# Performance work log

Hardware: AMD Instinct MI355X
Metric: run time of the kernel (lower is better)

The kernel has to match this reference:

```python
import jax, jax.numpy as jnp
import numpy as np

NEG_SLOPE = 0.2  # LeakyReLU slope used by PyG GATConv


def gat_conv(x, src, dst, W_src, W_dst, att_src, att_dst, bias, num_nodes):
    """Single-head PyG-style GATConv.
    x: [N, F_in]; src/dst: [E] int; W_*: [C, F_in]; att_*: [C]; bias: [C].
    """
    h_src = x @ W_src.T            # [N, C]
    h_dst = x @ W_dst.T            # [N, C]
    a_src = h_src @ att_src        # [N]
    a_dst = h_dst @ att_dst        # [N]
    e = a_src[src] + a_dst[dst]    # [E]
    e = jnp.where(e >= 0, e, NEG_SLOPE * e)  # leaky_relu
    # softmax over edges grouped by destination node
    m = jax.ops.segment_max(e, dst, num_segments=num_nodes)          # [N]
    ex = jnp.exp(e - m[dst])                                          # [E]
    denom = jax.ops.segment_sum(ex, dst, num_segments=num_nodes)      # [N]
    alpha = ex / (denom[dst] + 1e-16)                                 # [E]
    out = jax.ops.segment_sum(alpha[:, None] * h_src[src], dst,
                              num_segments=num_nodes)                 # [N, C]
    return out + bias


def setup_inputs() -> dict:
    key = jax.random.key(0)
    ks = jax.random.split(key, 16)
    N, E = 10000, 160000
    dim_in, dim_out = 4096, 20
    hid = dim_in // 4  # 1024
    x = jax.random.normal(ks[0], (N, dim_in), dtype=jnp.float32)
    edges = jax.random.randint(ks[1], (2, E), 0, N, dtype=jnp.int64)
    std = 0.01
    return {
        "x": x,
        "edges": edges,
        "W0": jax.random.normal(ks[2], (dim_out, dim_in)) * std,
        "b0": jnp.zeros((dim_out,), jnp.float32),
        "Ws1": jax.random.normal(ks[3], (hid, dim_in)) * (1.0 / np.sqrt(dim_in)),
        "Wd1": jax.random.normal(ks[4], (hid, dim_in)) * (1.0 / np.sqrt(dim_in)),
        "as1": jax.random.normal(ks[5], (hid,)) * 0.1,
        "ad1": jax.random.normal(ks[6], (hid,)) * 0.1,
        "b1": jnp.zeros((hid,), jnp.float32),
        "Ws2": jax.random.normal(ks[7], (dim_out, hid)) * (1.0 / np.sqrt(hid)),
        "Wd2": jax.random.normal(ks[8], (dim_out, hid)) * (1.0 / np.sqrt(hid)),
        "as2": jax.random.normal(ks[9], (dim_out,)) * 0.1,
        "ad2": jax.random.normal(ks[10], (dim_out,)) * 0.1,
        "b2": jnp.zeros((dim_out,), jnp.float32),
    }


def reference(x, edges, W0, b0, Ws1, Wd1, as1, ad1, b1, Ws2, Wd2, as2, ad2, b2):
    N = x.shape[0]
    # GATConv default add_self_loops=True; returned edge list includes them
    ar = jnp.arange(N, dtype=edges.dtype)
    new_edge = jnp.concatenate([edges, jnp.stack([ar, ar])], axis=1)  # [2, E+N]
    src, dst = new_edge[0], new_edge[1]

    # mil_score0: plain linear
    mil_score0 = x @ W0.T + b0                           # [N, dim_out]

    # mil_score1: two-layer GAT with ELU in between
    h = gat_conv(x, src, dst, Ws1, Wd1, as1, ad1, b1, N)  # [N, hid]
    h = jax.nn.elu(h)
    mil_score1 = gat_conv(h, src, dst, Ws2, Wd2, as2, ad2, b2, N)  # [N, dim_out]

    # softmax over proposals (dim=0) per class, fused with GAT output
    mil_score = jax.nn.softmax(mil_score0, axis=0) * mil_score1
    return (mil_score, new_edge)
```

## Files before the change

kernel.cpp:

```cpp
#include <hip/hip_runtime.h>

#define NN   10000
#define FIN  4096
#define HID  1024
#define CO   20
#define EE   160000
#define ET   170000
#define NBV  (HID + 22)

typedef __bf16 bf16x8 __attribute__((ext_vector_type(8)));
typedef float  f32x4  __attribute__((ext_vector_type(4)));

__device__ __forceinline__ float bf2f(unsigned short u) {
    unsigned int x = ((unsigned int)u) << 16;
    float f; __builtin_memcpy(&f, &x, 4); return f;
}
__device__ __forceinline__ unsigned short f2bf(float f) {
    unsigned int x; __builtin_memcpy(&x, &f, 4);
    unsigned int r = (x + 0x7fffu + ((x >> 16) & 1u)) >> 16;
    return (unsigned short)r;
}
__device__ __forceinline__ void unpack4(int2 v, float* f) {
    unsigned int a = (unsigned int)v.x, b = (unsigned int)v.y;
    f[0] = bf2f((unsigned short)(a & 0xffffu)); f[1] = bf2f((unsigned short)(a >> 16));
    f[2] = bf2f((unsigned short)(b & 0xffffu)); f[3] = bf2f((unsigned short)(b >> 16));
}
__device__ __forceinline__ int edge_at(const int* __restrict__ e, int idx, int is64) {
    return is64 ? e[2 * (size_t)idx] : e[idx];
}
__device__ __forceinline__ int4 pack8(float4 a, float4 b) {
    int4 o;
    o.x = (int)((unsigned)f2bf(a.x) | ((unsigned)f2bf(a.y) << 16));
    o.y = (int)((unsigned)f2bf(a.z) | ((unsigned)f2bf(a.w) << 16));
    o.z = (int)((unsigned)f2bf(b.x) | ((unsigned)f2bf(b.y) << 16));
    o.w = (int)((unsigned)f2bf(b.z) | ((unsigned)f2bf(b.w) << 16));
    return o;
}

__global__ void k_cast(const float* __restrict__ src, unsigned short* __restrict__ dst,
                       const int* __restrict__ edg, int* __restrict__ cnt,
                       int* __restrict__ flag) {
    int i = blockIdx.x * 256 + threadIdx.x;
    const float4* s = (const float4*)src + (size_t)i * 2;
    *(int4*)(dst + (size_t)i * 8) = pack8(s[0], s[1]);
    if (i < NN) cnt[i] = 0;
    if (i < 64) {
        int v = edg[2 * i + 1];
        unsigned long long bm = __ballot(v != 0);
        if (i == 0) flag[0] = (bm == 0ull) ? 1 : 0;
    }
}

#define BEXTB 2088
__global__ __launch_bounds__(256) void k_prep(const float* __restrict__ Ws1,
                                              const float* __restrict__ Wd1,
                                              const float* __restrict__ W0,
                                              const float* __restrict__ as1,
                                              const float* __restrict__ ad1,
                                              unsigned short* __restrict__ Bext,
                                              float* __restrict__ partS,
                                              float* __restrict__ partD) {
    if (blockIdx.x < BEXTB) {
        int i = blockIdx.x * 256 + threadIdx.x;
        int row = i >> 9;
        int col = (i & 511) * 8;
        const float* src = (row < HID) ? Ws1 + (size_t)row * FIN
                                       : W0 + (size_t)(row - HID) * FIN;
        const float4* s = (const float4*)(src + col);
        *(int4*)(Bext + (size_t)row * FIN + col) = pack8(s[0], s[1]);
    } else {
        int bx = blockIdx.x - BEXTB;
        int k = (bx & 15) * 256 + threadIdx.x;
        int chunk = bx >> 4;
        int r0 = chunk * 128;
        float s = 0.f, d = 0.f;
        for (int r = r0; r < r0 + 128; r++) {
            s += as1[r] * Ws1[(size_t)r * FIN + k];
            d += ad1[r] * Wd1[(size_t)r * FIN + k];
        }
        partS[chunk * FIN + k] = s;
        partD[chunk * FIN + k] = d;
    }
}

__global__ void k_vred(const float* __restrict__ partS, const float* __restrict__ partD,
                       const float* __restrict__ Wd2, const float* __restrict__ ad2,
                       unsigned short* __restrict__ Bext, float* __restrict__ wd2v) {
    int k = blockIdx.x * 256 + threadIdx.x;
    if (k < FIN) {
        float s = 0.f, d = 0.f;
        for (int j = 0; j < 8; j++) { s += partS[j * FIN + k]; d += partD[j * FIN + k]; }
        Bext[(size_t)(HID + CO) * FIN + k]     = f2bf(s);
        Bext[(size_t)(HID + CO + 1) * FIN + k] = f2bf(d);
    }
    if (k < HID) {
        float d2 = 0.f;
        for (int r = 0; r < CO; r++) d2 += ad2[r] * Wd2[(size_t)r * HID + k];
        wd2v[k] = d2;
    }
}

#define GBM 128
#define GBN 128
#define GBK 32
#define NMT ((NN + GBM - 1) / GBM)
#define NNT ((NBV + GBN - 1) / GBN)
#define NWG (NMT * NNT)

__global__ __launch_bounds__(256) void k_gemm_ext(
    const unsigned short* __restrict__ A, const unsigned short* __restrict__ B,
    unsigned short* __restrict__ H1, float* __restrict__ ext, int M) {
    __shared__ __bf16 As[2][GBM * GBK];
    __shared__ __bf16 Bs[2][GBN * GBK];
    int bid = blockIdx.x;
    int q = NWG >> 3, r = NWG & 7;
    int xcd = bid & 7, idx = bid >> 3;
    int swz = (xcd < r ? xcd * (q + 1) : r * (q + 1) + (xcd - r) * q) + idx;
    int mt = swz / NNT;
    int nt = swz - mt * NNT;
    int m0 = mt * GBM;
    int n0 = nt * GBN;
    int tid = threadIdx.x;
    int lane = tid & 63, wave = tid >> 6;
    int wm = (wave >> 1) * 64, wn = (wave & 1) * 64;
    int lrow = lane & 15, lk8 = (lane >> 4) * 8;

    int srow = lane >> 2;
    int scol = (lane & 3) * 8;
    int arow = wave * 32;
    int gmA0 = m0 + arow + srow;      if (gmA0 >= M) gmA0 = M - 1;
    int gmA1 = m0 + arow + 16 + srow; if (gmA1 >= M) gmA1 = M - 1;
    int gnB0 = n0 + arow + srow;      if (gnB0 >= NBV) gnB0 = NBV - 1;
    int gnB1 = n0 + arow + 16 + srow; if (gnB1 >= NBV) gnB1 = NBV - 1;
    const unsigned short* pA0 = A + (size_t)gmA0 * FIN + scol;
    const unsigned short* pA1 = A + (size_t)gmA1 * FIN + scol;
    const unsigned short* pB0 = B + (size_t)gnB0 * FIN + scol;
    const unsigned short* pB1 = B + (size_t)gnB1 * FIN + scol;

    f32x4 acc[4][4];
#pragma unroll
    for (int r2 = 0; r2 < 4; r2++)
#pragma unroll
        for (int c = 0; c < 4; c++) acc[r2][c] = (f32x4){0.f, 0.f, 0.f, 0.f};

    auto stage = [&](int buf, int k0) {
        __builtin_amdgcn_global_load_lds(
            (const __attribute__((address_space(1))) void*)(pA0 + k0),
            (__attribute__((address_space(3))) void*)&As[buf][arow * GBK], 16, 0, 0);
        __builtin_amdgcn_global_load_lds(
            (const __attribute__((address_space(1))) void*)(pA1 + k0),
            (__attribute__((address_space(3))) void*)&As[buf][(arow + 16) * GBK], 16, 0, 0);
        __builtin_amdgcn_global_load_lds(
            (const __attribute__((address_space(1))) void*)(pB0 + k0),
            (__attribute__((address_space(3))) void*)&Bs[buf][arow * GBK], 16, 0, 0);
        __builtin_amdgcn_global_load_lds(
            (const __attribute__((address_space(1))) void*)(pB1 + k0),
            (__attribute__((address_space(3))) void*)&Bs[buf][(arow + 16) * GBK], 16, 0, 0);
    };

    stage(0, 0);
    int cur = 0;
    for (int k0 = 0; k0 < FIN; k0 += GBK) {
        __syncthreads();
        if (k0 + GBK < FIN) stage(cur ^ 1, k0 + GBK);
        bf16x8 af[4], bfr[4];
#pragma unroll
        for (int r2 = 0; r2 < 4; r2++)
            af[r2] = *(const bf16x8*)(&As[cur][(wm + r2 * 16 + lrow) * GBK + lk8]);
#pragma unroll
        for (int c = 0; c < 4; c++)
            bfr[c] = *(const bf16x8*)(&Bs[cur][(wn + c * 16 + lrow) * GBK + lk8]);
#pragma unroll
        for (int r2 = 0; r2 < 4; r2++)
#pragma unroll
            for (int c = 0; c < 4; c++)
                acc[r2][c] = __builtin_amdgcn_mfma_f32_16x16x32_bf16(af[r2], bfr[c], acc[r2][c], 0, 0, 0);
        cur ^= 1;
    }
    int orow = (lane >> 4) * 4, ocol = lane & 15;
#pragma unroll
    for (int r2 = 0; r2 < 4; r2++)
#pragma unroll
        for (int c = 0; c < 4; c++)
#pragma unroll
            for (int i = 0; i < 4; i++) {
                int m = m0 + wm + r2 * 16 + orow + i;
                int n = n0 + wn + c * 16 + ocol;
                if (m < M) {
                    float v = acc[r2][c][i];
                    if (n < HID)      H1[(size_t)m * HID + n] = f2bf(v);
                    else if (n < NBV) ext[(size_t)(n - HID) * NN + m] = v;
                }
            }
}

#define CNTB 665
__global__ __launch_bounds__(256) void k_cfs(const int* __restrict__ edges,
                                             const int* __restrict__ flag,
                                             int* __restrict__ cnt,
                                             const float* __restrict__ ext,
                                             float* __restrict__ gmax,
                                             float* __restrict__ ginv) {
    if (blockIdx.x < CNTB) {
        int k = blockIdx.x * 256 + threadIdx.x;
        if (k >= ET) return;
        int is64 = flag[0];
        int d = (k < EE) ? edge_at(edges, EE + k, is64) : (k - EE);
        if ((unsigned)d < NN) atomicAdd(&cnt[d], 1);
    } else {
        int c = blockIdx.x - CNTB, t = threadIdx.x, lane = t & 63, wv = t >> 6;
        const float* row = ext + (size_t)c * NN;
        __shared__ float r4[4];
        __shared__ float bv;
        float m = -INFINITY;
        for (int n = t; n < NN; n += 256) m = fmaxf(m, row[n]);
        for (int o = 32; o; o >>= 1) m = fmaxf(m, __shfl_xor(m, o, 64));
        if (lane == 0) r4[wv] = m;
        __syncthreads();
        if (t == 0) bv = fmaxf(fmaxf(r4[0], r4[1]), fmaxf(r4[2], r4[3]));
        __syncthreads();
        float gm = bv;
        __syncthreads();
        float s = 0.f;
        for (int n = t; n < NN; n += 256) s += expf(row[n] - gm);
        for (int o = 32; o; o >>= 1) s += __shfl_xor(s, o, 64);
        if (lane == 0) r4[wv] = s;
        __syncthreads();
        if (t == 0) { gmax[c] = gm; ginv[c] = 1.0f / (r4[0] + r4[1] + r4[2] + r4[3]); }
    }
}

__global__ __launch_bounds__(1024) void k_scan(const int* __restrict__ cnt,
                                               int* __restrict__ offs,
                                               int* __restrict__ cursor) {
    int t = threadIdx.x, lane = t & 63, wv = t >> 6;
    int base = t * 10;
    int c[10]; int tot = 0;
    if (base < NN) {
#pragma unroll
        for (int j = 0; j < 10; j++) { c[j] = cnt[base + j]; tot += c[j]; }
    }
    int incl = tot;
#pragma unroll
    for (int o = 1; o < 64; o <<= 1) {
        int v = __shfl_up(incl, o, 64);
        if (lane >= o) incl += v;
    }
    __shared__ int wsum[16];
    if (lane == 63) wsum[wv] = incl;
    __syncthreads();
    if (t < 16) {
        int v = wsum[t];
        int inc2 = v;
#pragma unroll
        for (int o = 1; o < 16; o <<= 1) {
            int u = __shfl_up(inc2, o, 64);
            if (t >= o) inc2 += u;
        }
        wsum[t] = inc2 - v;
    }
    __syncthreads();
    int excl = incl - tot + wsum[wv];
    if (base < NN) {
        int run = excl;
#pragma unroll
        for (int j = 0; j < 10; j++) {
            cursor[base + j] = run;
            run += c[j];
            offs[base + j + 1] = run;
        }
    }
    if (t == 0) offs[0] = 0;
}

__global__ void k_scatter(const int* __restrict__ edges, const int* __restrict__ flag,
                          int* __restrict__ cursor, int* __restrict__ csr_src) {
    int k = blockIdx.x * 256 + threadIdx.x;
    if (k >= ET) return;
    int is64 = flag[0];
    int s, d;
    if (k < EE) { s = edge_at(edges, k, is64); d = edge_at(edges, EE + k, is64); }
    else        { s = d = k - EE; }
    if ((unsigned)d >= NN) return;
    if ((unsigned)s >= NN) s = 0;
    int pos = atomicAdd(&cursor[d], 1);
    csr_src[pos] = s;
}

__global__ __launch_bounds__(64) void k_agg1f(
    const int* __restrict__ offs, const int* __restrict__ csr,
    const float* __restrict__ a_src, const float* __restrict__ a_dst,
    const unsigned short* __restrict__ H1,
    const float* __restrict__ b1, const float* __restrict__ Ws2,
    const float* __restrict__ wd2v, const float* __restrict__ as2,
    float* __restrict__ H2, float* __restrict__ a_src2, float* __restrict__ a_dst2) {
    int n = blockIdx.x, lane = threadIdx.x;
    int b = offs[n], deg = offs[n + 1] - b;
    float ad = a_dst[n];
    __shared__ int   sc[128];
    __shared__ float av[128];
    bool small = (deg <= 128);
    float gm, inv;
    if (small) {
        float mymax = -INFINITY;
        for (int j = lane; j < deg; j += 64) {
            int s = csr[b + j];
            float v = a_src[s] + ad;
            v = (v >= 0.f) ? v : 0.2f * v;
            sc[j] = s; av[j] = v;
            mymax = fmaxf(mymax, v);
        }
        for (int o = 32; o; o >>= 1) mymax = fmaxf(mymax, __shfl_xor(mymax, o, 64));
        gm = mymax;
        float mysum = 0.f;
        for (int j = lane; j < deg; j += 64) {
            float e = expf(av[j] - gm);
            av[j] = e;
            mysum += e;
        }
        for (int o = 32; o; o >>= 1) mysum += __shfl_xor(mysum, o, 64);
        inv = 1.0f / (mysum + 1e-16f);
        for (int j = lane; j < deg; j += 64) av[j] *= inv;
        __syncthreads();
    } else {
        float mymax = -INFINITY;
        for (int j = lane; j < deg; j += 64) {
            float v = a_src[csr[b + j]] + ad;
            v = (v >= 0.f) ? v : 0.2f * v;
            mymax = fmaxf(mymax, v);
        }
        for (int o = 32; o; o >>= 1) mymax = fmaxf(mymax, __shfl_xor(mymax, o, 64));
        gm = mymax;
        float mysum = 0.f;
        for (int j = lane; j < deg; j += 64) {
            float v = a_src[csr[b + j]] + ad;
            v = (v >= 0.f) ? v : 0.2f * v;
            mysum += expf(v - gm);
        }
        for (int o = 32; o; o >>= 1) mysum += __shfl_xor(mysum, o, 64);
        inv = 1.0f / (mysum + 1e-16f);
    }
    float acc[16];
#pragma unroll
    for (int i = 0; i < 16; i++) acc[i] = 0.f;
    for (int base = 0; base < deg; base += 128) {
        int lim = deg - base; if (lim > 128) lim = 128;
        if (!small) {
            __syncthreads();
            for (int j = lane; j < lim; j += 64) {
                int s = csr[b + base + j];
                float v = a_src[s] + ad;
                v = (v >= 0.f) ? v : 0.2f * v;
                sc[j] = s; av[j] = expf(v - gm) * inv;
            }
            __syncthreads();
        }
        for (int j = 0; j < lim; j++) {
            int s = sc[j]; float w = av[j];
            const unsigned short* hp = H1 + (size_t)s * HID + lane * 8;
            int4 p0 = *(const int4*)hp;
            int4 p1 = *(const int4*)(hp + 512);
            float f[8];
            unpack4(make_int2(p0.x, p0.y), f);
            unpack4(make_int2(p0.z, p0.w), f + 4);
#pragma unroll
            for (int i = 0; i < 8; i++) acc[i] += w * f[i];
            unpack4(make_int2(p1.x, p1.y), f);
            unpack4(make_int2(p1.z, p1.w), f + 4);
#pragma unroll
            for (int i = 0; i < 8; i++) acc[8 + i] += w * f[i];
        }
    }
    float xf[16];
    {
        const float4* bp0 = (const float4*)(b1 + lane * 8);
        const float4* bp1 = (const float4*)(b1 + 512 + lane * 8);
        float4 c0 = bp0[0], c1 = bp0[1], c2 = bp1[0], c3 = bp1[1];
        float bb[16] = {c0.x,c0.y,c0.z,c0.w, c1.x,c1.y,c1.z,c1.w,
                        c2.x,c2.y,c2.z,c2.w, c3.x,c3.y,c3.z,c3.w};
#pragma unroll
        for (int i = 0; i < 16; i++) {
            float v = acc[i] + bb[i];
            xf[i] = (v > 0.f) ? v : (expf(v) - 1.f);
        }
    }
    float a2 = 0.f;
    for (int c = 0; c < 21; c++) {
        const float* wr = (c < CO) ? Ws2 + (size_t)c * HID : wd2v;
        const float4* w0 = (const float4*)(wr + lane * 8);
        const float4* w1 = (const float4*)(wr + 512 + lane * 8);
        float4 wa = w0[0], wb = w0[1], wc = w1[0], wd = w1[1];
        float dp = xf[0]*wa.x + xf[1]*wa.y + xf[2]*wa.z + xf[3]*wa.w
                 + xf[4]*wb.x + xf[5]*wb.y + xf[6]*wb.z + xf[7]*wb.w
                 + xf[8]*wc.x + xf[9]*wc.y + xf[10]*wc.z + xf[11]*wc.w
                 + xf[12]*wd.x + xf[13]*wd.y + xf[14]*wd.z + xf[15]*wd.w;
        for (int o = 32; o; o >>= 1) dp += __shfl_xor(dp, o, 64);
        if (c < CO) {
            if (lane == 0) H2[(size_t)n * CO + c] = dp;
            a2 += dp * as2[c];
        } else if (lane == 0) a_dst2[n] = dp;
    }
    if (lane == 0) a_src2[n] = a2;
}

__global__ __launch_bounds__(64) void k_agg2(const int* __restrict__ offs,
                                             const int* __restrict__ csr,
                                             const float* __restrict__ a_src,
                                             const float* __restrict__ a_dst,
                                             const float* __restrict__ H2,
                                             const float* __restrict__ b2,
                                             float* __restrict__ ms1T) {
    int n = blockIdx.x, lane = threadIdx.x;
    int b = offs[n], deg = offs[n + 1] - b;
    float ad = a_dst[n];
    __shared__ int   sc[128];
    __shared__ float av[128];
    bool small = (deg <= 128);
    float gm, inv;
    if (small) {
        float mymax = -INFINITY;
        for (int j = lane; j < deg; j += 64) {
            int s = csr[b + j];
            float v = a_src[s] + ad;
            v = (v >= 0.f) ? v : 0.2f * v;
            sc[j] = s; av[j] = v;
            mymax = fmaxf(mymax, v);
        }
        for (int o = 32; o; o >>= 1) mymax = fmaxf(mymax, __shfl_xor(mymax, o, 64));
        gm = mymax;
        float mysum = 0.f;
        for (int j = lane; j < deg; j += 64) {
            float e = expf(av[j] - gm);
            av[j] = e;
            mysum += e;
        }
        for (int o = 32; o; o >>= 1) mysum += __shfl_xor(mysum, o, 64);
        inv = 1.0f / (mysum + 1e-16f);
        for (int j = lane; j < deg; j += 64) av[j] *= inv;
        __syncthreads();
    } else {
        float mymax = -INFINITY;
        for (int j = lane; j < deg; j += 64) {
            float v = a_src[csr[b + j]] + ad;
            v = (v >= 0.f) ? v : 0.2f * v;
            mymax = fmaxf(mymax, v);
        }
        for (int o = 32; o; o >>= 1) mymax = fmaxf(mymax, __shfl_xor(mymax, o, 64));
        gm = mymax;
        float mysum = 0.f;
        for (int j = lane; j < deg; j += 64) {
            float v = a_src[csr[b + j]] + ad;
            v = (v >= 0.f) ? v : 0.2f * v;
            mysum += expf(v - gm);
        }
        for (int o = 32; o; o >>= 1) mysum += __shfl_xor(mysum, o, 64);
        inv = 1.0f / (mysum + 1e-16f);
    }
    int h = lane >> 5, c = lane & 31;
    float acc = 0.f;
    for (int base = 0; base < deg; base += 128) {
        int lim = deg - base; if (lim > 128) lim = 128;
        if (!small) {
            __syncthreads();
            for (int j = lane; j < lim; j += 64) {
                int s = csr[b + base + j];
                float v = a_src[s] + ad;
                v = (v >= 0.f) ? v : 0.2f * v;
                sc[j] = s; av[j] = expf(v - gm) * inv;
            }
            __syncthreads();
        }
        if (c < CO)
            for (int j = h; j < lim; j += 2)
                acc += av[j] * H2[(size_t)sc[j] * CO + c];
    }
    acc += __shfl_xor(acc, 32, 64);
    if (h == 0 && c < CO) ms1T[(size_t)c * NN + n] = acc + b2[c];
}

__global__ __launch_bounds__(256) void k_fout(const float* __restrict__ ext,
                                              const float* __restrict__ ms1T,
                                              const float* __restrict__ gmax,
                                              const float* __restrict__ ginv,
                                              const int* __restrict__ edges,
                                              const int* __restrict__ flag,
                                              float* __restrict__ out) {
    int g = blockIdx.x * 256 + threadIdx.x;
    if (g < NN) {
        float o[CO];
#pragma unroll
        for (int c = 0; c < CO; c++)
            o[c] = expf(ext[(size_t)c * NN + g] - gmax[c]) * ginv[c] * ms1T[(size_t)c * NN + g];
#pragma unroll
        for (int c = 0; c < CO; c += 4) {
            float4 v; v.x = o[c]; v.y = o[c + 1]; v.z = o[c + 2]; v.w = o[c + 3];
            *(float4*)(out + (size_t)g * CO + c) = v;
        }
    }
    if (g < ET) {
        int is64 = flag[0];
        int s, d;
        if (g < EE) { s = edge_at(edges, g, is64); d = edge_at(edges, EE + g, is64); }
        else        { s = d = g - EE; }
        out[NN * CO + g]      = bf2f(f2bf((float)s));
        out[NN * CO + ET + g] = bf2f(f2bf((float)d));
    }
}

extern "C" void kernel_launch(void* const* d_in, const int* in_sizes, int n_in,
                              void* d_out, int out_size, void* d_ws, size_t ws_size,
                              hipStream_t stream) {
    const float* x   = (const float*)d_in[0];
    const int*   edg = (const int*)d_in[1];
    const float* W0  = (const float*)d_in[2];
    const float* Ws1 = (const float*)d_in[4];
    const float* Wd1 = (const float*)d_in[5];
    const float* as1 = (const float*)d_in[6];
    const float* ad1 = (const float*)d_in[7];
    const float* b1  = (const float*)d_in[8];
    const float* Ws2 = (const float*)d_in[9];
    const float* Wd2 = (const float*)d_in[10];
    const float* as2 = (const float*)d_in[11];
    const float* ad2 = (const float*)d_in[12];
    const float* b2  = (const float*)d_in[13];
    float* out = (float*)d_out;

    char* p = (char*)d_ws;
    auto alloc = [&](size_t bytes) -> char* {
        char* r = p; p += (bytes + 511) & ~((size_t)511); return r;
    };
    unsigned short* xb   = (unsigned short*)alloc((size_t)NN * FIN * 2);
    unsigned short* Bext = (unsigned short*)alloc((size_t)NBV * FIN * 2);
    unsigned short* H1   = (unsigned short*)alloc((size_t)NN * HID * 2);
    float* ext    = (float*)alloc((size_t)22 * NN * 4);
    float* partS  = (float*)alloc((size_t)8 * FIN * 4);
    float* partD  = (float*)alloc((size_t)8 * FIN * 4);
    float* wd2v   = (float*)alloc(HID * 4);
    float* H2     = (float*)alloc((size_t)NN * CO * 4);
    float* ms1T   = (float*)alloc((size_t)CO * NN * 4);
    float* a_src2 = (float*)alloc(NN * 4);
    float* a_dst2 = (float*)alloc(NN * 4);
    int* csr_src  = (int*)alloc((size_t)ET * 4);
    int* cnt      = (int*)alloc(NN * 4);
    int* offs     = (int*)alloc((NN + 1) * 4);
    int* cursor   = (int*)alloc(NN * 4);
    int* eflag    = (int*)alloc(64);
    float* gmax   = (float*)alloc(CO * 4);
    float* ginv   = (float*)alloc(CO * 4);

    k_cast<<<NN * FIN / 8 / 256, 256, 0, stream>>>(x, xb, edg, cnt, eflag);
    k_prep<<<BEXTB + 128, 256, 0, stream>>>(Ws1, Wd1, W0, as1, ad1, Bext, partS, partD);
    k_vred<<<FIN / 256, 256, 0, stream>>>(partS, partD, Wd2, ad2, Bext, wd2v);
    k_gemm_ext<<<NWG, 256, 0, stream>>>(xb, Bext, H1, ext, NN);
    k_cfs<<<CNTB + CO, 256, 0, stream>>>(edg, eflag, cnt, ext, gmax, ginv);
    k_scan<<<1, 1024, 0, stream>>>(cnt, offs, cursor);
    k_scatter<<<(ET + 255) / 256, 256, 0, stream>>>(edg, eflag, cursor, csr_src);
    k_agg1f<<<NN, 64, 0, stream>>>(offs, csr_src, ext + 20 * NN, ext + 21 * NN, H1,
                                   b1, Ws2, wd2v, as2, H2, a_src2, a_dst2);
    k_agg2<<<NN, 64, 0, stream>>>(offs, csr_src, a_src2, a_dst2, H2, b2, ms1T);
    k_fout<<<(ET + 255) / 256, 256, 0, stream>>>(ext, ms1T, gmax, ginv, edg, eflag, out);
}
```

Before: 535.3 us.

## Merge cast and prep kernels, pack four nodes per block in aggregation

Merges the x cast kernel and the weight prep kernel into a single launch by splitting on block index. Both aggregation kernels now process four destination nodes per 256-thread block, one wave per node, with per-wave LDS buffers. Block-wide barriers are replaced by an lgkmcnt wait, since each wave only touches its own LDS slice. The edge loops are also unrolled by four (and by two in the second layer) so several gather loads are in flight at once. The aim is lower launch overhead, better occupancy and more memory parallelism, at the cost of relying on wave-local LDS ordering for correctness.

Measured after the change: 579.6 us. 8.3% more time.

```diff
diff --git a/kernel.cpp b/kernel.cpp
--- a/kernel.cpp
+++ b/kernel.cpp
@@ -36,23 +36,18 @@
     o.w = (int)((unsigned)f2bf(b.z) | ((unsigned)f2bf(b.w) << 16));
     return o;
 }
-
-__global__ void k_cast(const float* __restrict__ src, unsigned short* __restrict__ dst,
-                       const int* __restrict__ edg, int* __restrict__ cnt,
-                       int* __restrict__ flag) {
-    int i = blockIdx.x * 256 + threadIdx.x;
-    const float4* s = (const float4*)src + (size_t)i * 2;
-    *(int4*)(dst + (size_t)i * 8) = pack8(s[0], s[1]);
-    if (i < NN) cnt[i] = 0;
-    if (i < 64) {
-        int v = edg[2 * i + 1];
-        unsigned long long bm = __ballot(v != 0);
-        if (i == 0) flag[0] = (bm == 0ull) ? 1 : 0;
-    }
-}
-
+__device__ __forceinline__ void wave_lds_fence() {
+    asm volatile("s_waitcnt lgkmcnt(0)" ::: "memory");
+}
+
+#define CASTB 20000
 #define BEXTB 2088
-__global__ __launch_bounds__(256) void k_prep(const float* __restrict__ Ws1,
+__global__ __launch_bounds__(256) void k_cast(const float* __restrict__ x,
+                                              unsigned short* __restrict__ xb,
+                                              const int* __restrict__ edg,
+                                              int* __restrict__ cnt,
+                                              int* __restrict__ flag,
+                                              const float* __restrict__ Ws1,
                                               const float* __restrict__ Wd1,
                                               const float* __restrict__ W0,
                                               const float* __restrict__ as1,
@@ -60,8 +55,22 @@
                                               unsigned short* __restrict__ Bext,
                                               float* __restrict__ partS,
                                               float* __restrict__ partD) {
-    if (blockIdx.x < BEXTB) {
-        int i = blockIdx.x * 256 + threadIdx.x;
+    int bid = blockIdx.x, t = threadIdx.x;
+    if (bid < CASTB) {
+        int i = bid * 256 + t;
+        const float4* s = (const float4*)x + (size_t)i * 2;
+        *(int4*)(xb + (size_t)i * 8) = pack8(s[0], s[1]);
+        if (i < NN) cnt[i] = 0;
+        if (i < 64) {
+            int v = edg[2 * i + 1];
+            unsigned long long bm = __ballot(v != 0);
+            if (i == 0) flag[0] = (bm == 0ull) ? 1 : 0;
+        }
+        return;
+    }
+    int b2 = bid - CASTB;
+    if (b2 < BEXTB) {
+        int i = b2 * 256 + t;
         int row = i >> 9;
         int col = (i & 511) * 8;
         const float* src = (row < HID) ? Ws1 + (size_t)row * FIN
@@ -69,8 +78,8 @@
         const float4* s = (const float4*)(src + col);
         *(int4*)(Bext + (size_t)row * FIN + col) = pack8(s[0], s[1]);
     } else {
-        int bx = blockIdx.x - BEXTB;
-        int k = (bx & 15) * 256 + threadIdx.x;
+        int bx = b2 - BEXTB;
+        int k = (bx & 15) * 256 + t;
         int chunk = bx >> 4;
         int r0 = chunk * 128;
         float s = 0.f, d = 0.f;
@@ -287,18 +296,20 @@
     csr_src[pos] = s;
 }
 
-__global__ __launch_bounds__(64) void k_agg1f(
+__global__ __launch_bounds__(256) void k_agg1f(
     const int* __restrict__ offs, const int* __restrict__ csr,
     const float* __restrict__ a_src, const float* __restrict__ a_dst,
     const unsigned short* __restrict__ H1,
     const float* __restrict__ b1, const float* __restrict__ Ws2,
     const float* __restrict__ wd2v, const float* __restrict__ as2,
     float* __restrict__ H2, float* __restrict__ a_src2, float* __restrict__ a_dst2) {
-    int n = blockIdx.x, lane = threadIdx.x;
+    int t = threadIdx.x, lane = t & 63, wv = t >> 6;
+    int n = blockIdx.x * 4 + wv;
+    __shared__ int   sc_s[4][128];
+    __shared__ float av_s[4][128];
+    int* sc = sc_s[wv]; float* av = av_s[wv];
     int b = offs[n], deg = offs[n + 1] - b;
     float ad = a_dst[n];
-    __shared__ int   sc[128];
-    __shared__ float av[128];
     bool small = (deg <= 128);
     float gm, inv;
     if (small) {
@@ -321,7 +332,6 @@
         for (int o = 32; o; o >>= 1) mysum += __shfl_xor(mysum, o, 64);
         inv = 1.0f / (mysum + 1e-16f);
         for (int j = lane; j < deg; j += 64) av[j] *= inv;
-        __syncthreads();
     } else {
         float mymax = -INFINITY;
         for (int j = lane; j < deg; j += 64) {
@@ -346,27 +356,63 @@
     for (int base = 0; base < deg; base += 128) {
         int lim = deg - base; if (lim > 128) lim = 128;
         if (!small) {
-            __syncthreads();
+            wave_lds_fence();
             for (int j = lane; j < lim; j += 64) {
                 int s = csr[b + base + j];
                 float v = a_src[s] + ad;
                 v = (v >= 0.f) ? v : 0.2f * v;
                 sc[j] = s; av[j] = expf(v - gm) * inv;
             }
-            __syncthreads();
-        }
-        for (int j = 0; j < lim; j++) {
+        }
+        wave_lds_fence();
+        int j = 0;
+        for (; j + 4 <= lim; j += 4) {
+            int s0 = sc[j], s1 = sc[j + 1], s2 = sc[j + 2], s3 = sc[j + 3];
+            float w0 = av[j], w1 = av[j + 1], w2 = av[j + 2], w3 = av[j + 3];
+            const unsigned short* h0 = H1 + (size_t)s0 * HID + lane * 8;
+            const unsigned short* h1 = H1 + (size_t)s1 * HID + lane * 8;
+            const unsigned short* h2 = H1 + (size_t)s2 * HID + lane * 8;
+            const unsigned short* h3 = H1 + (size_t)s3 * HID + lane * 8;
+            int4 a0 = *(const int4*)h0, c0 = *(const int4*)(h0 + 512);
+            int4 a1 = *(const int4*)h1, c1 = *(const int4*)(h1 + 512);
+            int4 a2 = *(const int4*)h2, c2 = *(const int4*)(h2 + 512);
+            int4 a3 = *(const int4*)h3, c3 = *(const int4*)(h3 + 512);
+            float f[8];
+            unpack4(make_int2(a0.x, a0.y), f); unpack4(make_int2(a0.z, a0.w), f + 4);
+#pragma unroll
+            for (int i = 0; i < 8; i++) acc[i] += w0 * f[i];
+            unpack4(make_int2(c0.x, c0.y), f); unpack4(make_int2(c0.z, c0.w), f + 4);
+#pragma unroll
+            for (int i = 0; i < 8; i++) acc[8 + i] += w0 * f[i];
+            unpack4(make_int2(a1.x, a1.y), f); unpack4(make_int2(a1.z, a1.w), f + 4);
+#pragma unroll
+            for (int i = 0; i < 8; i++) acc[i] += w1 * f[i];
+            unpack4(make_int2(c1.x, c1.y), f); unpack4(make_int2(c1.z, c1.w), f + 4);
+#pragma unroll
+            for (int i = 0; i < 8; i++) acc[8 + i] += w1 * f[i];
+            unpack4(make_int2(a2.x, a2.y), f); unpack4(make_int2(a2.z, a2.w), f + 4);
+#pragma unroll
+            for (int i = 0; i < 8; i++) acc[i] += w2 * f[i];
+            unpack4(make_int2(c2.x, c2.y), f); unpack4(make_int2(c2.z, c2.w), f + 4);
+#pragma unroll
+            for (int i = 0; i < 8; i++) acc[8 + i] += w2 * f[i];
+            unpack4(make_int2(a3.x, a3.y), f); unpack4(make_int2(a3.z, a3.w), f + 4);
+#pragma unroll
+            for (int i = 0; i < 8; i++) acc[i] += w3 * f[i];
+            unpack4(make_int2(c3.x, c3.y), f); unpack4(make_int2(c3.z, c3.w), f + 4);
+#pragma unroll
+            for (int i = 0; i < 8; i++) acc[8 + i] += w3 * f[i];
+        }
+        for (; j < lim; j++) {
             int s = sc[j]; float w = av[j];
             const unsigned short* hp = H1 + (size_t)s * HID + lane * 8;
             int4 p0 = *(const int4*)hp;
             int4 p1 = *(const int4*)(hp + 512);
             float f[8];
-            unpack4(make_int2(p0.x, p0.y), f);
-            unpack4(make_int2(p0.z, p0.w), f + 4);
+            unpack4(make_int2(p0.x, p0.y), f); unpack4(make_int2(p0.z, p0.w), f + 4);
 #pragma unroll
             for (int i = 0; i < 8; i++) acc[i] += w * f[i];
-            unpack4(make_int2(p1.x, p1.y), f);
-            unpack4(make_int2(p1.z, p1.w), f + 4);
+            unpack4(make_int2(p1.x, p1.y), f); unpack4(make_int2(p1.z, p1.w), f + 4);
 #pragma unroll
             for (int i = 0; i < 8; i++) acc[8 + i] += w * f[i];
         }
@@ -403,18 +449,20 @@
     if (lane == 0) a_src2[n] = a2;
 }
 
-__global__ __launch_bounds__(64) void k_agg2(const int* __restrict__ offs,
-                                             const int* __restrict__ csr,
-                                             const float* __restrict__ a_src,
-                                             const float* __restrict__ a_dst,
-                                             const float* __restrict__ H2,
-                                             const float* __restrict__ b2,
-                                             float* __restrict__ ms1T) {
-    int n = blockIdx.x, lane = threadIdx.x;
+__global__ __launch_bounds__(256) void k_agg2(const int* __restrict__ offs,
+                                              const int* __restrict__ csr,
+                                              const float* __restrict__ a_src,
+                                              const float* __restrict__ a_dst,
+                                              const float* __restrict__ H2,
+                                              const float* __restrict__ b2,
+                                              float* __restrict__ ms1T) {
+    int t = threadIdx.x, lane = t & 63, wv = t >> 6;
+    int n = blockIdx.x * 4 + wv;
+    __shared__ int   sc_s[4][128];
+    __shared__ float av_s[4][128];
+    int* sc = sc_s[wv]; float* av = av_s[wv];
     int b = offs[n], deg = offs[n + 1] - b;
     float ad = a_dst[n];
-    __shared__ int   sc[128];
-    __shared__ float av[128];
     bool small = (deg <= 128);
     float gm, inv;
     if (small) {
@@ -437,7 +485,6 @@
         for (int o = 32; o; o >>= 1) mysum += __shfl_xor(mysum, o, 64);
         inv = 1.0f / (mysum + 1e-16f);
         for (int j = lane; j < deg; j += 64) av[j] *= inv;
-        __syncthreads();
     } else {
         float mymax = -INFINITY;
         for (int j = lane; j < deg; j += 64) {
@@ -461,18 +508,26 @@
     for (int base = 0; base < deg; base += 128) {
         int lim = deg - base; if (lim > 128) lim = 128;
         if (!small) {
-            __syncthreads();
+            wave_lds_fence();
             for (int j = lane; j < lim; j += 64) {
                 int s = csr[b + base + j];
                 float v = a_src[s] + ad;
                 v = (v >= 0.f) ? v : 0.2f * v;
                 sc[j] = s; av[j] = expf(v - gm) * inv;
             }
-            __syncthreads();
-        }
-        if (c < CO)
-            for (int j = h; j < lim; j += 2)
+        }
+        wave_lds_fence();
+        if (c < CO) {
+            int j = h;
+            for (; j + 2 < lim; j += 4) {
+                int s0 = sc[j], s1 = sc[j + 2];
+                float w0 = av[j], w1 = av[j + 2];
+                acc += w0 * H2[(size_t)s0 * CO + c];
+                acc += w1 * H2[(size_t)s1 * CO + c];
+            }
+            for (; j < lim; j += 2)
                 acc += av[j] * H2[(size_t)sc[j] * CO + c];
+        }
     }
     acc += __shfl_xor(acc, 32, 64);
     if (h == 0 && c < CO) ms1T[(size_t)c * NN + n] = acc + b2[c];
@@ -548,15 +603,16 @@
     float* gmax   = (float*)alloc(CO * 4);
     float* ginv   = (float*)alloc(CO * 4);
 
-    k_cast<<<NN * FIN / 8 / 256, 256, 0, stream>>>(x, xb, edg, cnt, eflag);
-    k_prep<<<BEXTB + 128, 256, 0, stream>>>(Ws1, Wd1, W0, as1, ad1, Bext, partS, partD);
+    k_cast<<<CASTB + BEXTB + 128, 256, 0, stream>>>(x, xb, edg, cnt, eflag,
+                                                    Ws1, Wd1, W0, as1, ad1,
+                                                    Bext, partS, partD);
     k_vred<<<FIN / 256, 256, 0, stream>>>(partS, partD, Wd2, ad2, Bext, wd2v);
     k_gemm_ext<<<NWG, 256, 0, stream>>>(xb, Bext, H1, ext, NN);
     k_cfs<<<CNTB + CO, 256, 0, stream>>>(edg, eflag, cnt, ext, gmax, ginv);
     k_scan<<<1, 1024, 0, stream>>>(cnt, offs, cursor);
     k_scatter<<<(ET + 255) / 256, 256, 0, stream>>>(edg, eflag, cursor, csr_src);
-    k_agg1f<<<NN, 64, 0, stream>>>(offs, csr_src, ext + 20 * NN, ext + 21 * NN, H1,
-                                   b1, Ws2, wd2v, as2, H2, a_src2, a_dst2);
-    k_agg2<<<NN, 64, 0, stream>>>(offs, csr_src, a_src2, a_dst2, H2, b2, ms1T);
+    k_agg1f<<<NN / 4, 256, 0, stream>>>(offs, csr_src, ext + 20 * NN, ext + 21 * NN, H1,
+                                        b1, Ws2, wd2v, as2, H2, a_src2, a_dst2);
+    k_agg2<<<NN / 4, 256, 0, stream>>>(offs, csr_src, a_src2, a_dst2, H2, b2, ms1T);
     k_fout<<<(ET + 255) / 256, 256, 0, stream>>>(ext, ms1T, gmax, ginv, edg, eflag, out);
 }
```

## Fuse degree count into prep, column softmax into scatter, final output into agg2

Applied to the files above, without the earlier changes.

Moves the destination-degree atomic counting into the weight-prep kernel, merges the column-softmax statistics and edge-list output writes into the scatter kernel, and folds the final softmax-times-GAT product into the second aggregation kernel. This removes two launches (k_cfs and k_fout) and the ms1T intermediate buffer round trip. The output writes from agg2 are now strided per node rather than coalesced float4 per thread, and the reordered schedule changes which work overlaps.

Result: no change. 531.0 us (-0.8%).

```diff
diff --git a/kernel.cpp b/kernel.cpp
--- a/kernel.cpp
+++ b/kernel.cpp
@@ -52,6 +52,7 @@
 }
 
 #define BEXTB 2088
+#define CNTB  665
 __global__ __launch_bounds__(256) void k_prep(const float* __restrict__ Ws1,
                                               const float* __restrict__ Wd1,
                                               const float* __restrict__ W0,
@@ -59,7 +60,10 @@
                                               const float* __restrict__ ad1,
                                               unsigned short* __restrict__ Bext,
                                               float* __restrict__ partS,
-                                              float* __restrict__ partD) {
+                                              float* __restrict__ partD,
+                                              const int* __restrict__ edges,
+                                              const int* __restrict__ flag,
+                                              int* __restrict__ cnt) {
     if (blockIdx.x < BEXTB) {
         int i = blockIdx.x * 256 + threadIdx.x;
         int row = i >> 9;
@@ -68,7 +72,7 @@
                                        : W0 + (size_t)(row - HID) * FIN;
         const float4* s = (const float4*)(src + col);
         *(int4*)(Bext + (size_t)row * FIN + col) = pack8(s[0], s[1]);
-    } else {
+    } else if (blockIdx.x < BEXTB + 128) {
         int bx = blockIdx.x - BEXTB;
         int k = (bx & 15) * 256 + threadIdx.x;
         int chunk = bx >> 4;
@@ -80,6 +84,12 @@
         }
         partS[chunk * FIN + k] = s;
         partD[chunk * FIN + k] = d;
+    } else {
+        int k = (blockIdx.x - BEXTB - 128) * 256 + threadIdx.x;
+        if (k >= ET) return;
+        int is64 = flag[0];
+        int d = (k < EE) ? edge_at(edges, EE + k, is64) : (k - EE);
+        if ((unsigned)d < NN) atomicAdd(&cnt[d], 1);
     }
 }
 
@@ -194,19 +204,70 @@
             }
 }
 
-#define CNTB 665
-__global__ __launch_bounds__(256) void k_cfs(const int* __restrict__ edges,
-                                             const int* __restrict__ flag,
-                                             int* __restrict__ cnt,
-                                             const float* __restrict__ ext,
-                                             float* __restrict__ gmax,
-                                             float* __restrict__ ginv) {
+__global__ __launch_bounds__(1024) void k_scan(const int* __restrict__ cnt,
+                                               int* __restrict__ offs,
+                                               int* __restrict__ cursor) {
+    int t = threadIdx.x, lane = t & 63, wv = t >> 6;
+    int base = t * 10;
+    int c[10]; int tot = 0;
+    if (base < NN) {
+#pragma unroll
+        for (int j = 0; j < 10; j++) { c[j] = cnt[base + j]; tot += c[j]; }
+    }
+    int incl = tot;
+#pragma unroll
+    for (int o = 1; o < 64; o <<= 1) {
+        int v = __shfl_up(incl, o, 64);
+        if (lane >= o) incl += v;
+    }
+    __shared__ int wsum[16];
+    if (lane == 63) wsum[wv] = incl;
+    __syncthreads();
+    if (t < 16) {
+        int v = wsum[t];
+        int inc2 = v;
+#pragma unroll
+        for (int o = 1; o < 16; o <<= 1) {
+            int u = __shfl_up(inc2, o, 64);
+            if (t >= o) inc2 += u;
+        }
+        wsum[t] = inc2 - v;
+    }
+    __syncthreads();
+    int excl = incl - tot + wsum[wv];
+    if (base < NN) {
+        int run = excl;
+#pragma unroll
+        for (int j = 0; j < 10; j++) {
+            cursor[base + j] = run;
+            run += c[j];
+            offs[base + j + 1] = run;
+        }
+    }
+    if (t == 0) offs[0] = 0;
+}
+
+__global__ __launch_bounds__(256) void k_scatter(const int* __restrict__ edges,
+                                                 const int* __restrict__ flag,
+                                                 int* __restrict__ cursor,
+                                                 int* __restrict__ csr_src,
+                                                 const float* __restrict__ ext,
+                                                 float* __restrict__ gmax,
+                                                 float* __restrict__ ginv,
+                                                 float* __restrict__ out) {
     if (blockIdx.x < CNTB) {
         int k = blockIdx.x * 256 + threadIdx.x;
         if (k >= ET) return;
         int is64 = flag[0];
-        int d = (k < EE) ? edge_at(edges, EE + k, is64) : (k - EE);
-        if ((unsigned)d < NN) atomicAdd(&cnt[d], 1);
+        int s, d;
+        if (k < EE) { s = edge_at(edges, k, is64); d = edge_at(edges, EE + k, is64); }
+        else        { s = d = k - EE; }
+        out[NN * CO + k]      = bf2f(f2bf((float)s));
+        out[NN * CO + ET + k] = bf2f(f2bf((float)d));
+        if ((unsigned)d >= NN) return;
+        if ((unsigned)s >= NN) s = 0;
+        int pos = atomicAdd(&cursor[d], 1);
+        csr_src[pos] = s;
     } else {
         int c = blockIdx.x - CNTB, t = threadIdx.x, lane = t & 63, wv = t >> 6;
         const float* row = ext + (size_t)c * NN;
@@ -228,63 +289,6 @@
         __syncthreads();
         if (t == 0) { gmax[c] = gm; ginv[c] = 1.0f / (r4[0] + r4[1] + r4[2] + r4[3]); }
     }
-}
-
-__global__ __launch_bounds__(1024) void k_scan(const int* __restrict__ cnt,
-                                               int* __restrict__ offs,
-                                               int* __restrict__ cursor) {
-    int t = threadIdx.x, lane = t & 63, wv = t >> 6;
-    int base = t * 10;
-    int c[10]; int tot = 0;
-    if (base < NN) {
-#pragma unroll
-        for (int j = 0; j < 10; j++) { c[j] = cnt[base + j]; tot += c[j]; }
-    }
-    int incl = tot;
-#pragma unroll
-    for (int o = 1; o < 64; o <<= 1) {
-        int v = __shfl_up(incl, o, 64);
-        if (lane >= o) incl += v;
-    }
-    __shared__ int wsum[16];
-    if (lane == 63) wsum[wv] = incl;
-    __syncthreads();
-    if (t < 16) {
-        int v = wsum[t];
-        int inc2 = v;
-#pragma unroll
-        for (int o = 1; o < 16; o <<= 1) {
-            int u = __shfl_up(inc2, o, 64);
-            if (t >= o) inc2 += u;
-        }
-        wsum[t] = inc2 - v;
-    }
-    __syncthreads();
-    int excl = incl - tot + wsum[wv];
-    if (base < NN) {
-        int run = excl;
-#pragma unroll
-        for (int j = 0; j < 10; j++) {
-            cursor[base + j] = run;
-            run += c[j];
-            offs[base + j + 1] = run;
-        }
-    }
-    if (t == 0) offs[0] = 0;
-}
-
-__global__ void k_scatter(const int* __restrict__ edges, const int* __restrict__ flag,
-                          int* __restrict__ cursor, int* __restrict__ csr_src) {
-    int k = blockIdx.x * 256 + threadIdx.x;
-    if (k >= ET) return;
-    int is64 = flag[0];
-    int s, d;
-    if (k < EE) { s = edge_at(edges, k, is64); d = edge_at(edges, EE + k, is64); }
-    else        { s = d = k - EE; }
-    if ((unsigned)d >= NN) return;
-    if ((unsigned)s >= NN) s = 0;
-    int pos = atomicAdd(&cursor[d], 1);
-    csr_src[pos] = s;
 }
 
 __global__ __launch_bounds__(64) void k_agg1f(
@@ -409,7 +413,10 @@
                                              const float* __restrict__ a_dst,
                                              const float* __restrict__ H2,
                                              const float* __restrict__ b2,
-                                             float* __restrict__ ms1T) {
+                                             const float* __restrict__ ext,
+                                             const float* __restrict__ gmax,
+                                             const float* __restrict__ ginv,
+                                             float* __restrict__ out) {
     int n = blockIdx.x, lane = threadIdx.x;
     int b = offs[n], deg = offs[n + 1] - b;
     float ad = a_dst[n];
@@ -475,35 +482,10 @@
                 acc += av[j] * H2[(size_t)sc[j] * CO + c];
     }
     acc += __shfl_xor(acc, 32, 64);
-    if (h == 0 && c < CO) ms1T[(size_t)c * NN + n] = acc + b2[c];
-}
-
-__global__ __launch_bounds__(256) void k_fout(const float* __restrict__ ext,
-                                              const float* __restrict__ ms1T,
-                                              const float* __restrict__ gmax,
-                                              const float* __restrict__ ginv,
-                                              const int* __restrict__ edges,
-                                              const int* __restrict__ flag,
-                                              float* __restrict__ out) {
-    int g = blockIdx.x * 256 + threadIdx.x;
-    if (g < NN) {
-        float o[CO];
-#pragma unroll
-        for (int c = 0; c < CO; c++)
-            o[c] = expf(ext[(size_t)c * NN + g] - gmax[c]) * ginv[c] * ms1T[(size_t)c * NN + g];
-#pragma unroll
-        for (int c = 0; c < CO; c += 4) {
-            float4 v; v.x = o[c]; v.y = o[c + 1]; v.z = o[c + 2]; v.w = o[c + 3];
-            *(float4*)(out + (size_t)g * CO + c) = v;
-        }
-    }
-    if (g < ET) {
-        int is64 = flag[0];
-        int s, d;
-        if (g < EE) { s = edge_at(edges, g, is64); d = edge_at(edges, EE + g, is64); }
-        else        { s = d = g - EE; }
-        out[NN * CO + g]      = bf2f(f2bf((float)s));
-        out[NN * CO + ET + g] = bf2f(f2bf((float)d));
+    if (h == 0 && c < CO) {
+        float ms1 = acc + b2[c];
+        float o = expf(ext[(size_t)c * NN + n] - gmax[c]) * ginv[c] * ms1;
+        out[(size_t)n * CO + c] = o;
     }
 }
 
@@ -537,7 +519,6 @@
     float* partD  = (float*)alloc((size_t)8 * FIN * 4);
     float* wd2v   = (float*)alloc(HID * 4);
     float* H2     = (float*)alloc((size_t)NN * CO * 4);
-    float* ms1T   = (float*)alloc((size_t)CO * NN * 4);
     float* a_src2 = (float*)alloc(NN * 4);
     float* a_dst2 = (float*)alloc(NN * 4);
     int* csr_src  = (int*)alloc((size_t)ET * 4);
@@ -549,14 +530,15 @@
     float* ginv   = (float*)alloc(CO * 4);
 
     k_cast<<<NN * FIN / 8 / 256, 256, 0, stream>>>(x, xb, edg, cnt, eflag);
-    k_prep<<<BEXTB + 128, 256, 0, stream>>>(Ws1, Wd1, W0, as1, ad1, Bext, partS, partD);
+    k_prep<<<BEXTB + 128 + CNTB, 256, 0, stream>>>(Ws1, Wd1, W0, as1, ad1,
+                                                   Bext, partS, partD, edg, eflag, cnt);
     k_vred<<<FIN / 256, 256, 0, stream>>>(partS, partD, Wd2, ad2, Bext, wd2v);
     k_gemm_ext<<<NWG, 256, 0, stream>>>(xb, Bext, H1, ext, NN);
-    k_cfs<<<CNTB + CO, 256, 0, stream>>>(edg, eflag, cnt, ext, gmax, ginv);
     k_scan<<<1, 1024, 0, stream>>>(cnt, offs, cursor);
-    k_scatter<<<(ET + 255) / 256, 256, 0, stream>>>(edg, eflag, cursor, csr_src);
+    k_scatter<<<CNTB + CO, 256, 0, stream>>>(edg, eflag, cursor, csr_src,
+                                             ext, gmax, ginv, out);
     k_agg1f<<<NN, 64, 0, stream>>>(offs, csr_src, ext + 20 * NN, ext + 21 * NN, H1,
                                    b1, Ws2, wd2v, as2, H2, a_src2, a_dst2);
-    k_agg2<<<NN, 64, 0, stream>>>(offs, csr_src, a_src2, a_dst2, H2, b2, ms1T);
-    k_fout<<<(ET + 255) / 256, 256, 0, stream>>>(ext, ms1T, gmax, ginv, edg, eflag, out);
-}
+    k_agg2<<<NN, 64, 0, stream>>>(offs, csr_src, a_src2, a_dst2, H2, b2,
+                                  ext, gmax, ginv, out);
+}
```
